# Performance work log

Measured on AMD Instinct MI355X. Metric: run time of the kernel, lower is better.

Reference implementation:

```python
import jax, jax.numpy as jnp
import numpy as np

N_NODES = 100000
N_EDGES = 640000
H_FEATS = 128


def setup_inputs() -> dict:
    key = jax.random.key(0)
    k_h, k_src, k_dst, k_w1, k_b1, k_w2, k_b2 = jax.random.split(key, 7)
    h = jax.random.normal(k_h, (N_NODES, H_FEATS), dtype=jnp.float32)
    src = jax.random.randint(k_src, (N_EDGES,), 0, N_NODES, dtype=jnp.int64)
    dst = jax.random.randint(k_dst, (N_EDGES,), 0, N_NODES, dtype=jnp.int64)
    # nn.Linear params: W1 (h_feats, 2*h_feats) as (out, in); store transposed for x @ W
    lim1 = 1.0 / np.sqrt(2 * H_FEATS)
    W1 = jax.random.uniform(k_w1, (2 * H_FEATS, H_FEATS), jnp.float32, -lim1, lim1)
    b1 = jax.random.uniform(k_b1, (H_FEATS,), jnp.float32, -lim1, lim1)
    lim2 = 1.0 / np.sqrt(H_FEATS)
    W2 = jax.random.uniform(k_w2, (H_FEATS, 1), jnp.float32, -lim2, lim2)
    b2 = jax.random.uniform(k_b2, (1,), jnp.float32, -lim2, lim2)
    return {"h": h, "src": src, "dst": dst, "W1": W1, "b1": b1, "W2": W2, "b2": b2}


def reference(h, src, dst, W1, b1, W2, b2):
    # gather src/dst node features per edge and concat: [E, 2*h_feats]
    he = jnp.concatenate([h[src], h[dst]], axis=1)
    hidden = jax.nn.relu(he @ W1 + b1)          # [E, h_feats]
    score = (hidden @ W2 + b2)[:, 0]            # [E]
    return score
```

## Files before the change

### kernel.cpp

```cpp
#include <hip/hip_runtime.h>

#define N_NODES 100000
#define N_EDGES 640000
#define F 128
#define NT 6250
#define NBLK 512

typedef __attribute__((ext_vector_type(8))) short short8;
typedef __attribute__((ext_vector_type(4))) float float4v;

static __device__ __forceinline__ unsigned short f2bf(float f) {
    unsigned int u = __float_as_uint(f);
    u += 0x7fffu + ((u >> 16) & 1u);
    return (unsigned short)(u >> 16);
}

__global__ __launch_bounds__(256) void prep_wt(
    const float* __restrict__ W1, unsigned short* __restrict__ Wt)
{
    int id = blockIdx.x * 256 + threadIdx.x;
    int n = id >> 7, k = id & 127;
    float v = W1[((n & 128) + k) * 128 + (n & 127)];
    Wt[id] = f2bf(v);
}

__global__ __launch_bounds__(256, 2) void node_proj(
    const float* __restrict__ h, const unsigned short* __restrict__ Wt,
    const float* __restrict__ b1,
    unsigned short* __restrict__ A, unsigned short* __restrict__ B)
{
    __shared__ unsigned short w_lds[256 * 136];
    __shared__ unsigned short h_lds[2][16 * 136];

    const int tid  = threadIdx.x;
    const int lane = tid & 63;
    const int l16  = lane & 15;
    const int quad = lane >> 4;
    const int w    = tid >> 6;

#pragma unroll
    for (int i = 0; i < 16; ++i) {
        int c = i * 256 + tid;
        int r = c >> 4, cc = c & 15;
        uint4 v = *(const uint4*)(Wt + (size_t)r * F + cc * 8);
        *(uint4*)&w_lds[r * 136 + cc * 8] = v;
    }

    const bool isA = (w < 2);
    float4 bv[4];
#pragma unroll
    for (int p = 0; p < 4; ++p) {
        int col = (w & 1) * 64 + p * 16 + quad * 4;
        bv[p] = isA ? *(const float4*)(b1 + col) : make_float4(0.f, 0.f, 0.f, 0.f);
    }
    unsigned short* outp = isA ? A : B;
    const int colb = (w & 1) * 64;

    int srow[2], sc4[2];
#pragma unroll
    for (int i = 0; i < 2; ++i) { int f = i * 256 + tid; srow[i] = f >> 5; sc4[i] = f & 31; }

#define LOADH(PF, T)                                                           \
    _Pragma("unroll") for (int i = 0; i < 2; ++i)                              \
        PF[i] = *(const float4*)(h + ((size_t)(T) * 16 + srow[i]) * F + sc4[i] * 4);

#define CVTWRITE(PF, DST)                                                      \
    _Pragma("unroll") for (int i = 0; i < 2; ++i) {                            \
        uint2 p;                                                               \
        p.x = (unsigned)f2bf(PF[i].x) | ((unsigned)f2bf(PF[i].y) << 16);       \
        p.y = (unsigned)f2bf(PF[i].z) | ((unsigned)f2bf(PF[i].w) << 16);       \
        *(uint2*)&(DST)[srow[i] * 136 + sc4[i] * 4] = p;                       \
    }

    int t = blockIdx.x;
    float4 pf[2];
    if (t < NT) { LOADH(pf, t); CVTWRITE(pf, h_lds[0]); }
    __syncthreads();

    int cur = 0;
    while (t < NT) {
        const int tn = t + NBLK;
        const bool actn = (tn < NT);
        if (actn) LOADH(pf, tn);

        const unsigned short* hb = h_lds[cur];
        float4v acc[4];
#pragma unroll
        for (int p = 0; p < 4; ++p) acc[p] = (float4v){0.f, 0.f, 0.f, 0.f};
#pragma unroll
        for (int k0 = 0; k0 < 4; ++k0) {
            const int kb = k0 * 32 + quad * 8;
            short8 bf = *(const short8*)&hb[l16 * 136 + kb];
#pragma unroll
            for (int p = 0; p < 4; ++p) {
                short8 af = *(const short8*)&w_lds[(w * 64 + p * 16 + l16) * 136 + kb];
                acc[p] = __builtin_amdgcn_mfma_f32_16x16x32_bf16(af, bf, acc[p], 0, 0, 0);
            }
        }

        if (actn) CVTWRITE(pf, h_lds[cur ^ 1]);

        {
            const size_t nodeoff = ((size_t)t * 16 + l16) * F;
#pragma unroll
            for (int p = 0; p < 4; ++p) {
                ushort4 sv;
                sv.x = f2bf(acc[p][0] + bv[p].x);
                sv.y = f2bf(acc[p][1] + bv[p].y);
                sv.z = f2bf(acc[p][2] + bv[p].z);
                sv.w = f2bf(acc[p][3] + bv[p].w);
                *(ushort4*)(outp + nodeoff + colb + p * 16 + quad * 4) = sv;
            }
        }
        __syncthreads();
        cur ^= 1; t = tn;
    }
#undef LOADH
#undef CVTWRITE
}

__global__ __launch_bounds__(256) void edge_score(
    const unsigned short* __restrict__ A, const unsigned short* __restrict__ B,
    const int* __restrict__ src, const int* __restrict__ dst,
    const float* __restrict__ W2, const float* __restrict__ b2,
    float* __restrict__ out)
{
    const int tid = threadIdx.x;
    const int sub = tid & 7;
    const int e0  = blockIdx.x * 128 + (tid >> 3) * 4;
    const int j0  = sub * 16;

    const int4 sv = *(const int4*)(src + e0);
    const int4 dv = *(const int4*)(dst + e0);
    const int s[4] = {sv.x, sv.y, sv.z, sv.w};
    const int d[4] = {dv.x, dv.y, dv.z, dv.w};

    uint4 av0[4], av1[4], bv0[4], bv1[4];
#pragma unroll
    for (int i = 0; i < 4; ++i) {
        const uint4* Ap = (const uint4*)(A + (size_t)s[i] * F + j0);
        const uint4* Bp = (const uint4*)(B + (size_t)d[i] * F + j0);
        av0[i] = Ap[0]; av1[i] = Ap[1];
        bv0[i] = Bp[0]; bv1[i] = Bp[1];
    }

    const float4* Wp = (const float4*)(W2 + j0);
    const float4 w0 = Wp[0], w1 = Wp[1], w2 = Wp[2], w3 = Wp[3];
    const float bias = b2[0];

#define TERM(UA, UB, WL, WH)                                                   \
    {                                                                          \
        float fa0 = __uint_as_float((UA) << 16);                               \
        float fa1 = __uint_as_float((UA) & 0xFFFF0000u);                       \
        float fb0 = __uint_as_float((UB) << 16);                               \
        float fb1 = __uint_as_float((UB) & 0xFFFF0000u);                       \
        sacc = fmaf(fmaxf(fa0 + fb0, 0.f), (WL), sacc);                        \
        sacc = fmaf(fmaxf(fa1 + fb1, 0.f), (WH), sacc);                        \
    }
#pragma unroll
    for (int i = 0; i < 4; ++i) {
        float sacc = 0.f;
        TERM(av0[i].x, bv0[i].x, w0.x, w0.y)
        TERM(av0[i].y, bv0[i].y, w0.z, w0.w)
        TERM(av0[i].z, bv0[i].z, w1.x, w1.y)
        TERM(av0[i].w, bv0[i].w, w1.z, w1.w)
        TERM(av1[i].x, bv1[i].x, w2.x, w2.y)
        TERM(av1[i].y, bv1[i].y, w2.z, w2.w)
        TERM(av1[i].z, bv1[i].z, w3.x, w3.y)
        TERM(av1[i].w, bv1[i].w, w3.z, w3.w)
        sacc += __shfl_xor(sacc, 1);
        sacc += __shfl_xor(sacc, 2);
        sacc += __shfl_xor(sacc, 4);
        if (sub == 0) out[e0 + i] = sacc + bias;
    }
#undef TERM
}

extern "C" void kernel_launch(void* const* d_in, const int* in_sizes, int n_in,
                              void* d_out, int out_size, void* d_ws, size_t ws_size,
                              hipStream_t stream) {
    const float* h   = (const float*)d_in[0];
    const int*   src = (const int*)d_in[1];
    const int*   dst = (const int*)d_in[2];
    const float* W1  = (const float*)d_in[3];
    const float* b1  = (const float*)d_in[4];
    const float* W2  = (const float*)d_in[5];
    const float* b2  = (const float*)d_in[6];
    float* out = (float*)d_out;

    unsigned short* Wt = (unsigned short*)d_ws;
    unsigned short* A  = Wt + 256 * 128;
    unsigned short* B  = A + (size_t)N_NODES * F;

    prep_wt<<<128, 256, 0, stream>>>(W1, Wt);
    node_proj<<<NBLK, 256, 0, stream>>>(h, Wt, b1, A, B);
    edge_score<<<N_EDGES / 128, 256, 0, stream>>>(A, B, src, dst, W2, b2, out);
}
```

Measured before the change: 160.7 us.

## Stage node projection outputs through LDS, swizzle weights, and interleave edge gathers

node_proj now stores W in an XOR-swizzled LDS layout instead of a padded one, which frees space. It drops the double-buffered h tile and stages the bf16 A/B outputs in LDS, so each row is written to global memory as full 16-byte coalesced stores rather than scattered 8-byte writes. This adds an extra barrier per tile and serialises the h prefetch conversion behind the compute. edge_score changes which 16-byte chunks each lane reads (sub*8 and 64+sub*8), so adjacent lanes touch adjacent addresses, with W2 indexed to match.

```diff
diff --git a/kernel.cpp b/kernel.cpp
--- a/kernel.cpp
+++ b/kernel.cpp
@@ -29,8 +29,10 @@
     const float* __restrict__ b1,
     unsigned short* __restrict__ A, unsigned short* __restrict__ B)
 {
-    __shared__ unsigned short w_lds[256 * 136];
-    __shared__ unsigned short h_lds[2][16 * 136];
+    __shared__ unsigned short w_swz[256 * 128];
+    __shared__ unsigned short hb[16 * 136];
+    __shared__ unsigned short oA[16 * 136];
+    __shared__ unsigned short oB[16 * 136];
 
     const int tid  = threadIdx.x;
     const int lane = tid & 63;
@@ -40,21 +42,21 @@
 
 #pragma unroll
     for (int i = 0; i < 16; ++i) {
-        int c = i * 256 + tid;
-        int r = c >> 4, cc = c & 15;
-        uint4 v = *(const uint4*)(Wt + (size_t)r * F + cc * 8);
-        *(uint4*)&w_lds[r * 136 + cc * 8] = v;
+        int cl = i * 256 + tid;
+        int r = cl >> 4, c = cl & 15;
+        uint4 v = *(const uint4*)(Wt + (size_t)r * F + c * 8);
+        *(uint4*)&w_swz[((r << 4) + (c ^ (r & 15))) * 8] = v;
     }
 
     const bool isA = (w < 2);
+    const int colb = (w & 1) * 64;
     float4 bv[4];
 #pragma unroll
     for (int p = 0; p < 4; ++p) {
-        int col = (w & 1) * 64 + p * 16 + quad * 4;
+        int col = colb + p * 16 + quad * 4;
         bv[p] = isA ? *(const float4*)(b1 + col) : make_float4(0.f, 0.f, 0.f, 0.f);
     }
-    unsigned short* outp = isA ? A : B;
-    const int colb = (w & 1) * 64;
+    unsigned short* ostage = isA ? oA : oB;
 
     int srow[2], sc4[2];
 #pragma unroll
@@ -64,56 +66,59 @@
     _Pragma("unroll") for (int i = 0; i < 2; ++i)                              \
         PF[i] = *(const float4*)(h + ((size_t)(T) * 16 + srow[i]) * F + sc4[i] * 4);
 
-#define CVTWRITE(PF, DST)                                                      \
+#define CVTWRITE(PF)                                                           \
     _Pragma("unroll") for (int i = 0; i < 2; ++i) {                            \
         uint2 p;                                                               \
         p.x = (unsigned)f2bf(PF[i].x) | ((unsigned)f2bf(PF[i].y) << 16);       \
         p.y = (unsigned)f2bf(PF[i].z) | ((unsigned)f2bf(PF[i].w) << 16);       \
-        *(uint2*)&(DST)[srow[i] * 136 + sc4[i] * 4] = p;                       \
+        *(uint2*)&hb[srow[i] * 136 + sc4[i] * 4] = p;                          \
     }
 
     int t = blockIdx.x;
     float4 pf[2];
-    if (t < NT) { LOADH(pf, t); CVTWRITE(pf, h_lds[0]); }
+    LOADH(pf, t); CVTWRITE(pf);
     __syncthreads();
 
-    int cur = 0;
     while (t < NT) {
         const int tn = t + NBLK;
         const bool actn = (tn < NT);
         if (actn) LOADH(pf, tn);
 
-        const unsigned short* hb = h_lds[cur];
         float4v acc[4];
 #pragma unroll
         for (int p = 0; p < 4; ++p) acc[p] = (float4v){0.f, 0.f, 0.f, 0.f};
 #pragma unroll
         for (int k0 = 0; k0 < 4; ++k0) {
-            const int kb = k0 * 32 + quad * 8;
-            short8 bf = *(const short8*)&hb[l16 * 136 + kb];
+            short8 bf = *(const short8*)&hb[l16 * 136 + k0 * 32 + quad * 8];
+            const int cc = (k0 * 4 + quad);
 #pragma unroll
             for (int p = 0; p < 4; ++p) {
-                short8 af = *(const short8*)&w_lds[(w * 64 + p * 16 + l16) * 136 + kb];
+                const int row = w * 64 + p * 16 + l16;
+                short8 af = *(const short8*)&w_swz[((row << 4) + (cc ^ l16)) * 8];
                 acc[p] = __builtin_amdgcn_mfma_f32_16x16x32_bf16(af, bf, acc[p], 0, 0, 0);
             }
         }
-
-        if (actn) CVTWRITE(pf, h_lds[cur ^ 1]);
-
-        {
-            const size_t nodeoff = ((size_t)t * 16 + l16) * F;
-#pragma unroll
-            for (int p = 0; p < 4; ++p) {
-                ushort4 sv;
-                sv.x = f2bf(acc[p][0] + bv[p].x);
-                sv.y = f2bf(acc[p][1] + bv[p].y);
-                sv.z = f2bf(acc[p][2] + bv[p].z);
-                sv.w = f2bf(acc[p][3] + bv[p].w);
-                *(ushort4*)(outp + nodeoff + colb + p * 16 + quad * 4) = sv;
-            }
+        __syncthreads();
+
+        if (actn) CVTWRITE(pf);
+#pragma unroll
+        for (int p = 0; p < 4; ++p) {
+            ushort4 sv;
+            sv.x = f2bf(acc[p][0] + bv[p].x);
+            sv.y = f2bf(acc[p][1] + bv[p].y);
+            sv.z = f2bf(acc[p][2] + bv[p].z);
+            sv.w = f2bf(acc[p][3] + bv[p].w);
+            *(ushort4*)&ostage[l16 * 136 + colb + p * 16 + quad * 4] = sv;
         }
         __syncthreads();
-        cur ^= 1; t = tn;
+
+        {
+            const int r = tid >> 4, c = tid & 15;
+            const size_t goff = ((size_t)t * 16 + r) * F + c * 8;
+            *(uint4*)(A + goff) = *(const uint4*)&oA[r * 136 + c * 8];
+            *(uint4*)(B + goff) = *(const uint4*)&oB[r * 136 + c * 8];
+        }
+        t = tn;
     }
 #undef LOADH
 #undef CVTWRITE
@@ -128,7 +133,6 @@
     const int tid = threadIdx.x;
     const int sub = tid & 7;
     const int e0  = blockIdx.x * 128 + (tid >> 3) * 4;
-    const int j0  = sub * 16;
 
     const int4 sv = *(const int4*)(src + e0);
     const int4 dv = *(const int4*)(dst + e0);
@@ -138,14 +142,18 @@
     uint4 av0[4], av1[4], bv0[4], bv1[4];
 #pragma unroll
     for (int i = 0; i < 4; ++i) {
-        const uint4* Ap = (const uint4*)(A + (size_t)s[i] * F + j0);
-        const uint4* Bp = (const uint4*)(B + (size_t)d[i] * F + j0);
-        av0[i] = Ap[0]; av1[i] = Ap[1];
-        bv0[i] = Bp[0]; bv1[i] = Bp[1];
-    }
-
-    const float4* Wp = (const float4*)(W2 + j0);
-    const float4 w0 = Wp[0], w1 = Wp[1], w2 = Wp[2], w3 = Wp[3];
+        const unsigned short* Ar = A + (size_t)s[i] * F;
+        const unsigned short* Br = B + (size_t)d[i] * F;
+        av0[i] = *(const uint4*)(Ar + sub * 8);
+        av1[i] = *(const uint4*)(Ar + 64 + sub * 8);
+        bv0[i] = *(const uint4*)(Br + sub * 8);
+        bv1[i] = *(const uint4*)(Br + 64 + sub * 8);
+    }
+
+    const float4 w0 = *(const float4*)(W2 + sub * 8);
+    const float4 w1 = *(const float4*)(W2 + sub * 8 + 4);
+    const float4 w2 = *(const float4*)(W2 + 64 + sub * 8);
+    const float4 w3 = *(const float4*)(W2 + 64 + sub * 8 + 4);
     const float bias = b2[0];
 
 #define TERM(UA, UB, WL, WH)                                                   \
```

Result: faster. 155.0 us (median of 2 runs) (-3.6%).
